# Kernel tuning notes

Hardware: AMD Instinct MI355X
Metric: run time of the kernel (lower is better)

## Reference

```python
import jax, jax.numpy as jnp
import numpy as np

N = 10000      # nodes
E = 160000     # edges
G = 512        # graphs in batch
IN, H, OUT = 128, 512, 16
L = 4          # num_layers
EPS = 1e-5


def setup_inputs() -> dict:
    key = jax.random.key(0)
    ks = jax.random.split(key, 8)
    x = jax.random.normal(ks[0], (N, IN), dtype=jnp.float32)
    edge_index = jax.random.randint(ks[1], (2, E), 0, N)
    batch = jnp.sort(jax.random.randint(ks[2], (N,), 0, G))
    # GCNConv layer 0 (IN -> H) and layers 1..L-1 (H -> H), plus per-layer LayerNorm affine
    W0 = jax.random.normal(ks[3], (IN, H), dtype=jnp.float32) / np.float32(np.sqrt(IN))
    b0 = jnp.zeros((H,), jnp.float32)
    g0 = jnp.ones((IN,), jnp.float32)
    be0 = jnp.zeros((IN,), jnp.float32)
    Wh = jax.random.normal(ks[4], (L - 1, H, H), dtype=jnp.float32) / np.float32(np.sqrt(H))
    bh = jnp.zeros((L - 1, H), jnp.float32)
    gh = jnp.ones((L - 1, H), jnp.float32)
    beh = jnp.zeros((L - 1, H), jnp.float32)
    linW = jax.random.normal(ks[5], (H, OUT), dtype=jnp.float32) / np.float32(np.sqrt(H))
    linb = jnp.zeros((OUT,), jnp.float32)
    return dict(x=x, edge_index=edge_index, batch=batch, W0=W0, b0=b0, g0=g0, be0=be0,
                Wh=Wh, bh=bh, gh=gh, beh=beh, linW=linW, linb=linb)


def _layernorm(x, g, b):
    mu = jnp.mean(x, axis=-1, keepdims=True)
    var = jnp.var(x, axis=-1, keepdims=True)
    return (x - mu) * jax.lax.rsqrt(var + EPS) * g + b


def _gcn(x, W, b, src, dst, dinv):
    # GCNConv with self-loops: out_i = sum_{j->i} d_j^-1/2 d_i^-1/2 (xW)_j + d_i^-1 (xW)_i + b
    h = x @ W                                   # [N, H']
    coef = (dinv[src] * dinv[dst])[:, None]     # [E, 1]
    agg = jax.ops.segment_sum(h[src] * coef, dst, num_segments=N)
    agg = agg + h * (dinv * dinv)[:, None]      # self-loop term
    return agg + b


def reference(x, edge_index, batch, W0, b0, g0, be0, Wh, bh, gh, beh, linW, linb):
    src, dst = edge_index[0], edge_index[1]
    # degree with self-loops (counted on destination nodes, edge weight 1)
    deg = jax.ops.segment_sum(jnp.ones((E,), x.dtype), dst, num_segments=N) + 1.0
    dinv = jax.lax.rsqrt(deg)
    h = jax.nn.relu(_gcn(_layernorm(x, g0, be0), W0, b0, src, dst, dinv))
    for i in range(L - 1):
        h = jax.nn.relu(_gcn(_layernorm(h, gh[i], beh[i]), Wh[i], bh[i], src, dst, dinv))
    # scatter-mean pooling by graph id
    counts = jax.ops.segment_sum(jnp.ones((N,), x.dtype), batch, num_segments=G)
    pooled = jax.ops.segment_sum(h, batch, num_segments=G) / jnp.maximum(counts, 1.0)[:, None]
    return pooled @ linW + linb
```

## Files before the change

kernel.cpp:

```cpp
#include <hip/hip_runtime.h>

#define NN 10000
#define NE 160000
#define NG 512
#define DIN 128
#define DH 512
#define DOUT 16
#define NPAD 10112

typedef __bf16 bf16_t;
typedef __attribute__((ext_vector_type(8))) __bf16 bf16x8;
typedef __attribute__((ext_vector_type(2))) __bf16 bf16x2;
typedef __attribute__((ext_vector_type(4))) float f32x4;
typedef __attribute__((ext_vector_type(2))) float f32x2;

#define LNB 2500
#define DEGB ((NE + 255) / 256)
#define WTE (512 * DIN + 3 * DH * DH)
#define WTB ((WTE + 255) / 256)
#define CURB ((NN + 255) / 256)


__global__ __launch_bounds__(256) void k_prep(const float* __restrict__ x,
                                              const float* __restrict__ g0,
                                              const float* __restrict__ be0,
                                              bf16_t* __restrict__ lnx,
                                              const int* __restrict__ dst,
                                              int* __restrict__ deg,
                                              const float* __restrict__ W0,
                                              const float* __restrict__ Wh,
                                              bf16_t* __restrict__ Wt0,
                                              bf16_t* __restrict__ Wth,
                                              int* __restrict__ cursor) {
    int b = blockIdx.x;
    int tid = threadIdx.x;
    if (b < LNB) {
        int row = b * 4 + (tid >> 6);
        int lane = tid & 63;
        const float* xr = x + (size_t)row * DIN;
        float v0 = xr[lane], v1 = xr[lane + 64];
        float s = v0 + v1, s2 = v0 * v0 + v1 * v1;
#pragma unroll
        for (int off = 32; off; off >>= 1) {
            s += __shfl_xor(s, off);
            s2 += __shfl_xor(s2, off);
        }
        float mu = s * (1.f / 128.f);
        float var = s2 * (1.f / 128.f) - mu * mu;
        float r = rsqrtf(var + 1e-5f);
        bf16_t* yr = lnx + (size_t)row * DIN;
        yr[lane] = (bf16_t)((v0 - mu) * r * g0[lane] + be0[lane]);
        yr[lane + 64] = (bf16_t)((v1 - mu) * r * g0[lane + 64] + be0[lane + 64]);
    } else if (b < LNB + DEGB) {
        int e = (b - LNB) * 256 + tid;
        if (e < NE) atomicAdd(&deg[dst[e]], 1);
    } else if (b < LNB + DEGB + WTB) {
        int idx = (b - LNB - DEGB) * 256 + tid;
        if (idx < 512 * DIN) {
            int k = idx >> 9, n = idx & 511;
            Wt0[n * DIN + k] = (bf16_t)W0[idx];
        } else if (idx < WTE) {
            int j = idx - 512 * DIN;
            int l = j >> 18;
            int r2 = j & 262143;
            int k = r2 >> 9, n = r2 & 511;
            Wth[((size_t)l << 18) + n * DH + k] = (bf16_t)Wh[j];
        }
    } else {
        int i = (b - LNB - DEGB - WTB) * 256 + tid;
        if (i < NN) cursor[i] = 0;
    }
}


__global__ __launch_bounds__(1024) void k_scan(const int* __restrict__ cnt,
                                               int* __restrict__ rowptr,
                                               float* __restrict__ dinv) {
    __shared__ int part[1024];
    int tid = threadIdx.x;
    const int PER = 10;
    int base = tid * PER;
    int local[PER];
    int s = 0;
#pragma unroll
    for (int i = 0; i < PER; ++i) {
        int idx = base + i;
        int v = (idx < NN) ? cnt[idx] : 0;
        if (idx < NN) dinv[idx] = rsqrtf((float)v + 1.0f);
        local[i] = s;
        s += v;
    }
    part[tid] = s;
    __syncthreads();
    for (int off = 1; off < 1024; off <<= 1) {
        int v = (tid >= off) ? part[tid - off] : 0;
        __syncthreads();
        part[tid] += v;
        __syncthreads();
    }
    int offset = (tid > 0) ? part[tid - 1] : 0;
#pragma unroll
    for (int i = 0; i < PER; ++i) {
        int idx = base + i;
        if (idx < NN) rowptr[idx] = offset + local[i];
    }
    if (tid == 1023) rowptr[NN] = part[1023];
}

__global__ void k_fill_csr(const int* __restrict__ src, const int* __restrict__ dst,
                           const float* __restrict__ dinv, const int* __restrict__ rowptr,
                           int* __restrict__ cursor, int2* __restrict__ csr) {
    int e = blockIdx.x * blockDim.x + threadIdx.x;
    if (e >= NE) return;
    int s = src[e], d = dst[e];
    int pos = atomicAdd(&cursor[d], 1);
    csr[rowptr[d] + pos] = make_int2(s, __float_as_int(dinv[s] * dinv[d]));
}


__global__ __launch_bounds__(256) void k_ln512(const bf16_t* __restrict__ x,
                                               const float* __restrict__ g,
                                               const float* __restrict__ b,
                                               bf16_t* __restrict__ y) {
    int row = blockIdx.x * 4 + (threadIdx.x >> 6);
    int lane = threadIdx.x & 63;
    if (row >= NN) return;
    int c0 = lane * 8;
    bf16x8 v = *(const bf16x8*)&x[(size_t)row * DH + c0];
    float f[8];
    float s = 0.f, s2 = 0.f;
#pragma unroll
    for (int i = 0; i < 8; ++i) {
        f[i] = (float)v[i];
        s += f[i];
        s2 += f[i] * f[i];
    }
#pragma unroll
    for (int off = 32; off; off >>= 1) {
        s += __shfl_xor(s, off);
        s2 += __shfl_xor(s2, off);
    }
    float mu = s * (1.f / 512.f);
    float var = s2 * (1.f / 512.f) - mu * mu;
    float r = rsqrtf(var + 1e-5f);
    f32x4 g0 = *(const f32x4*)&g[c0], g1 = *(const f32x4*)&g[c0 + 4];
    f32x4 b0 = *(const f32x4*)&b[c0], b1 = *(const f32x4*)&b[c0 + 4];
    bf16x8 o;
#pragma unroll
    for (int i = 0; i < 4; ++i) {
        o[i] = (bf16_t)((f[i] - mu) * r * g0[i] + b0[i]);
        o[i + 4] = (bf16_t)((f[i + 4] - mu) * r * g1[i] + b1[i]);
    }
    *(bf16x8*)&y[(size_t)row * DH + c0] = o;
}


template <bool EPI>
__global__ __launch_bounds__(256) void k_gemm64(const bf16_t* __restrict__ A,
                                                const bf16_t* __restrict__ Bt,
                                                const float* __restrict__ bias,
                                                bf16_t* __restrict__ C, int K) {
    __shared__ bf16_t As[64 * 64];
    __shared__ bf16_t Bs[64 * 64];
    int tid = threadIdx.x;
    int lane = tid & 63, w = tid >> 6;
    int row0 = blockIdx.x * 64, col0 = blockIdx.y * 64;
    int wm = w >> 1, wn = w & 1;

    f32x4 acc[2][2];
#pragma unroll
    for (int i = 0; i < 2; ++i)
#pragma unroll
        for (int j = 0; j < 2; ++j) acc[i][j] = (f32x4){0.f, 0.f, 0.f, 0.f};

    int lr = lane >> 3;
    int lc = lane & 7;

    for (int kt = 0; kt < K; kt += 64) {
#pragma unroll
        for (int i = 0; i < 2; ++i) {
            int r = w * 16 + i * 8 + lr;
            int cg = lc ^ (r & 7);
            const bf16_t* srca = A + (size_t)(row0 + r) * K + kt + cg * 8;
            __builtin_amdgcn_global_load_lds(
                (const __attribute__((address_space(1))) void*)srca,
                (__attribute__((address_space(3))) void*)(As + (w * 16 + i * 8) * 64),
                16, 0, 0);
            const bf16_t* srcb = Bt + (size_t)(col0 + r) * K + kt + cg * 8;
            __builtin_amdgcn_global_load_lds(
                (const __attribute__((address_space(1))) void*)srcb,
                (__attribute__((address_space(3))) void*)(Bs + (w * 16 + i * 8) * 64),
                16, 0, 0);
        }
        __syncthreads();
#pragma unroll
        for (int ks = 0; ks < 2; ++ks) {
            bf16x8 af[2], bfr[2];
#pragma unroll
            for (int mi = 0; mi < 2; ++mi) {
                int mr = wm * 32 + mi * 16 + (lane & 15);
                int c = (ks * 4 + (lane >> 4)) ^ (mr & 7);
                af[mi] = *(const bf16x8*)&As[mr * 64 + c * 8];
            }
#pragma unroll
            for (int ni = 0; ni < 2; ++ni) {
                int nr = wn * 32 + ni * 16 + (lane & 15);
                int c = (ks * 4 + (lane >> 4)) ^ (nr & 7);
                bfr[ni] = *(const bf16x8*)&Bs[nr * 64 + c * 8];
            }
#pragma unroll
            for (int mi = 0; mi < 2; ++mi)
#pragma unroll
                for (int ni = 0; ni < 2; ++ni)
                    acc[mi][ni] = __builtin_amdgcn_mfma_f32_16x16x32_bf16(
                        af[mi], bfr[ni], acc[mi][ni], 0, 0, 0);
        }
        __syncthreads();
    }
#pragma unroll
    for (int mi = 0; mi < 2; ++mi)
#pragma unroll
        for (int ni = 0; ni < 2; ++ni) {
            int col = col0 + wn * 32 + ni * 16 + (lane & 15);
            float bv = EPI ? bias[col] : 0.f;
#pragma unroll
            for (int q = 0; q < 4; ++q) {
                int row = row0 + wm * 32 + mi * 16 + (lane >> 4) * 4 + q;
                float v = acc[mi][ni][q];
                if (EPI) v = fmaxf(v + bv, 0.f);
                C[(size_t)row * DH + col] = (bf16_t)v;
            }
        }
}


__global__ __launch_bounds__(256) void k_agg128(const bf16_t* __restrict__ H,
                                                const int* __restrict__ rowptr,
                                                const int2* __restrict__ csr,
                                                const float* __restrict__ dinv,
                                                bf16_t* __restrict__ out) {
    __shared__ float part[4][DIN];
    int n = blockIdx.x;
    int w = threadIdx.x >> 6, lane = threadIdx.x & 63;
    int c0 = lane * 2;
    float a0 = 0.f, a1 = 0.f;
    int s0 = rowptr[n], s1 = rowptr[n + 1];
    int k = s0 + w;
    for (; k + 4 < s1; k += 8) {
        int2 eA = csr[k], eB = csr[k + 4];
        float cA = __int_as_float(eA.y), cB = __int_as_float(eB.y);
        bf16x2 vA = *(const bf16x2*)&H[(size_t)eA.x * DIN + c0];
        bf16x2 vB = *(const bf16x2*)&H[(size_t)eB.x * DIN + c0];
        a0 += (float)vA[0] * cA + (float)vB[0] * cB;
        a1 += (float)vA[1] * cA + (float)vB[1] * cB;
    }
    if (k < s1) {
        int2 eA = csr[k];
        float cA = __int_as_float(eA.y);
        bf16x2 vA = *(const bf16x2*)&H[(size_t)eA.x * DIN + c0];
        a0 += (float)vA[0] * cA;
        a1 += (float)vA[1] * cA;
    }
    part[w][c0] = a0;
    part[w][c0 + 1] = a1;
    __syncthreads();
    if (threadIdx.x < 64) {
        int cc = threadIdx.x * 2;
        float b0 = part[0][cc] + part[1][cc] + part[2][cc] + part[3][cc];
        float b1 = part[0][cc + 1] + part[1][cc + 1] + part[2][cc + 1] + part[3][cc + 1];
        float di = dinv[n], sc = di * di;
        bf16x2 vs = *(const bf16x2*)&H[(size_t)n * DIN + cc];
        b0 += (float)vs[0] * sc;
        b1 += (float)vs[1] * sc;
        bf16x2 o;
        o[0] = (bf16_t)b0;
        o[1] = (bf16_t)b1;
        *(bf16x2*)&out[(size_t)n * DIN + cc] = o;
    }
}


template <bool DO_LN>
__global__ __launch_bounds__(256) void k_agg(const bf16_t* __restrict__ H,
                                             const int* __restrict__ rowptr,
                                             const int2* __restrict__ csr,
                                             const float* __restrict__ dinv,
                                             const float* __restrict__ bias,
                                             const float* __restrict__ gamma,
                                             const float* __restrict__ beta,
                                             bf16_t* __restrict__ out) {
    __shared__ float part[4][DH];
    __shared__ float rs[8];
    int n = blockIdx.x;
    int w = threadIdx.x >> 6, lane = threadIdx.x & 63;
    int c0 = lane * 8;
    float acc[8] = {0.f, 0.f, 0.f, 0.f, 0.f, 0.f, 0.f, 0.f};
    int s0 = rowptr[n], s1 = rowptr[n + 1];
    int k = s0 + w;
    for (; k + 4 < s1; k += 8) {
        int2 eA = csr[k], eB = csr[k + 4];
        float cA = __int_as_float(eA.y), cB = __int_as_float(eB.y);
        bf16x8 vA = *(const bf16x8*)&H[(size_t)eA.x * DH + c0];
        bf16x8 vB = *(const bf16x8*)&H[(size_t)eB.x * DH + c0];
#pragma unroll
        for (int i = 0; i < 8; ++i) acc[i] += (float)vA[i] * cA + (float)vB[i] * cB;
    }
    if (k < s1) {
        int2 eA = csr[k];
        float cA = __int_as_float(eA.y);
        bf16x8 vA = *(const bf16x8*)&H[(size_t)eA.x * DH + c0];
#pragma unroll
        for (int i = 0; i < 8; ++i) acc[i] += (float)vA[i] * cA;
    }
    *(f32x4*)&part[w][c0] = (f32x4){acc[0], acc[1], acc[2], acc[3]};
    *(f32x4*)&part[w][c0 + 4] = (f32x4){acc[4], acc[5], acc[6], acc[7]};
    __syncthreads();
    int cc = threadIdx.x * 2;
    f32x2 p0 = *(const f32x2*)&part[0][cc];
    f32x2 p1 = *(const f32x2*)&part[1][cc];
    f32x2 p2 = *(const f32x2*)&part[2][cc];
    f32x2 p3 = *(const f32x2*)&part[3][cc];
    float a0 = p0[0] + p1[0] + p2[0] + p3[0];
    float a1 = p0[1] + p1[1] + p2[1] + p3[1];
    float di = dinv[n], sc = di * di;
    bf16x2 vs = *(const bf16x2*)&H[(size_t)n * DH + cc];
    a0 += (float)vs[0] * sc;
    a1 += (float)vs[1] * sc;
    a0 = fmaxf(a0 + bias[cc], 0.f);
    a1 = fmaxf(a1 + bias[cc + 1], 0.f);
    bf16x2 o;
    if (DO_LN) {
        float s = a0 + a1, s2 = a0 * a0 + a1 * a1;
#pragma unroll
        for (int off = 32; off; off >>= 1) {
            s += __shfl_xor(s, off);
            s2 += __shfl_xor(s2, off);
        }
        if (lane == 0) {
            rs[w] = s;
            rs[4 + w] = s2;
        }
        __syncthreads();
        s = rs[0] + rs[1] + rs[2] + rs[3];
        s2 = rs[4] + rs[5] + rs[6] + rs[7];
        float mu = s * (1.f / 512.f);
        float var = s2 * (1.f / 512.f) - mu * mu;
        float r = rsqrtf(var + 1e-5f);
        o[0] = (bf16_t)((a0 - mu) * r * gamma[cc] + beta[cc]);
        o[1] = (bf16_t)((a1 - mu) * r * gamma[cc + 1] + beta[cc + 1]);
    } else {
        o[0] = (bf16_t)a0;
        o[1] = (bf16_t)a1;
    }
    *(bf16x2*)&out[(size_t)n * DH + cc] = o;
}


__global__ __launch_bounds__(256) void k_poolfin(const bf16_t* __restrict__ h,
                                                 const int* __restrict__ batch,
                                                 const float* __restrict__ linW,
                                                 const float* __restrict__ linb,
                                                 float* __restrict__ out) {
    __shared__ float pooled[DH];
    __shared__ float red[256];
    int g = blockIdx.x;
    int t = threadIdx.x;
    int lo = 0, hi = NN;
    while (lo < hi) {
        int mid = (lo + hi) >> 1;
        if (batch[mid] < g) lo = mid + 1;
        else hi = mid;
    }
    int start = lo;
    hi = NN;
    while (lo < hi) {
        int mid = (lo + hi) >> 1;
        if (batch[mid] < g + 1) lo = mid + 1;
        else hi = mid;
    }
    int end = lo;
    int c0 = t * 2;
    float a0 = 0.f, a1 = 0.f;
    for (int i = start; i < end; ++i) {
        bf16x2 v = *(const bf16x2*)&h[(size_t)i * DH + c0];
        a0 += (float)v[0];
        a1 += (float)v[1];
    }
    float inv = 1.f / fmaxf((float)(end - start), 1.0f);
    pooled[c0] = a0 * inv;
    pooled[c0 + 1] = a1 * inv;
    __syncthreads();
    int o = t & 15, c = t >> 4;
    float s = 0.f;
    int k0 = c * 32;
    for (int k = k0; k < k0 + 32; ++k) s += pooled[k] * linW[k * DOUT + o];
    red[t] = s;
    __syncthreads();
    if (t < DOUT) {
        float acc2 = 0.f;
        for (int cc = 0; cc < 16; ++cc) acc2 += red[cc * 16 + t];
        out[g * DOUT + t] = acc2 + linb[t];
    }
}


extern "C" void kernel_launch(void* const* d_in, const int* in_sizes, int n_in,
                              void* d_out, int out_size, void* d_ws, size_t ws_size,
                              hipStream_t stream) {
    const float* x = (const float*)d_in[0];
    const int* ei = (const int*)d_in[1];
    const int* batch = (const int*)d_in[2];
    const float* W0 = (const float*)d_in[3];
    const float* b0 = (const float*)d_in[4];
    const float* g0 = (const float*)d_in[5];
    const float* be0 = (const float*)d_in[6];
    const float* Wh = (const float*)d_in[7];
    const float* bh = (const float*)d_in[8];
    const float* gh = (const float*)d_in[9];
    const float* beh = (const float*)d_in[10];
    const float* linW = (const float*)d_in[11];
    const float* linb = (const float*)d_in[12];
    float* out = (float*)d_out;

    bf16_t* lnbuf = (bf16_t*)d_ws;
    bf16_t* Cbf = lnbuf + (size_t)NPAD * DH;
    bf16_t* lnx = Cbf + (size_t)NPAD * DH;
    bf16_t* aggx = lnx + (size_t)NPAD * DIN;
    bf16_t* Wt0 = aggx + (size_t)NPAD * DIN;
    bf16_t* Wth = Wt0 + 512 * DIN;
    float* dinv = (float*)(Wth + 3 * DH * DH);
    int* deg = (int*)(dinv + NN);
    int* rowptr = deg + NN;
    int* cursor = rowptr + NN + 1;
    int2* csr = (int2*)(cursor + NN + 1);

    const int* srcp = ei;
    const int* dstp = ei + NE;

    hipMemsetAsync(deg, 0, NN * sizeof(int), stream);
    k_prep<<<LNB + DEGB + WTB + CURB, 256, 0, stream>>>(x, g0, be0, lnx, dstp, deg,
                                                        W0, Wh, Wt0, Wth, cursor);
    k_scan<<<1, 1024, 0, stream>>>(deg, rowptr, dinv);
    k_fill_csr<<<(NE + 255) / 256, 256, 0, stream>>>(srcp, dstp, dinv, rowptr, cursor, csr);

    dim3 gemm_grid(NPAD / 64, DH / 64);

    k_agg128<<<NN, 256, 0, stream>>>(lnx, rowptr, csr, dinv, aggx);
    k_gemm64<true><<<gemm_grid, 256, 0, stream>>>(aggx, Wt0, b0, Cbf, DIN);
    k_ln512<<<(NN + 3) / 4, 256, 0, stream>>>(Cbf, gh + 0 * DH, beh + 0 * DH, lnbuf);

    for (int l = 0; l < 2; ++l) {
        k_gemm64<false><<<gemm_grid, 256, 0, stream>>>(lnbuf, Wth + (size_t)l * DH * DH,
                                                       nullptr, Cbf, DH);
        k_agg<true><<<NN, 256, 0, stream>>>(Cbf, rowptr, csr, dinv, bh + l * DH,
                                            gh + (l + 1) * DH, beh + (l + 1) * DH, lnbuf);
    }
    k_gemm64<false><<<gemm_grid, 256, 0, stream>>>(lnbuf, Wth + (size_t)2 * DH * DH,
                                                   nullptr, Cbf, DH);
    k_agg<false><<<NN, 256, 0, stream>>>(Cbf, rowptr, csr, dinv, bh + 2 * DH,
                                         nullptr, nullptr, lnbuf);

    k_poolfin<<<NG, 256, 0, stream>>>(lnbuf, batch, linW, linb, out);
}
```

Measured before the change: 207.4 us.

## Fuse final aggregation with pooling, enlarge GEMM tile, and optimise scan and gather unroll

The last aggregation now scatter-adds its ReLU outputs straight into a per-graph pooled buffer with float atomics, so the separate sequential pooling pass over node rows is gone. The buffer is zeroed by extra blocks in the prep kernel. The GEMM tile grows from 64x64 to 128x64 to get more reuse per block, at the cost of fewer blocks. The single-block scan switches from a shared-memory Hillis-Steele loop to wave shuffles, and the edge-gather loops unroll by four instead of two. The atomics make the pooled sums order-nondeterministic.

```diff
diff --git a/kernel.cpp b/kernel.cpp
--- a/kernel.cpp
+++ b/kernel.cpp
@@ -19,6 +19,7 @@
 #define WTE (512 * DIN + 3 * DH * DH)
 #define WTB ((WTE + 255) / 256)
 #define CURB ((NN + 255) / 256)
+#define PLB 256
 
 
 __global__ __launch_bounds__(256) void k_prep(const float* __restrict__ x,
@@ -31,7 +32,8 @@
                                               const float* __restrict__ Wh,
                                               bf16_t* __restrict__ Wt0,
                                               bf16_t* __restrict__ Wth,
-                                              int* __restrict__ cursor) {
+                                              int* __restrict__ cursor,
+                                              float* __restrict__ pooled) {
     int b = blockIdx.x;
     int tid = threadIdx.x;
     if (b < LNB) {
@@ -66,9 +68,12 @@
             int k = r2 >> 9, n = r2 & 511;
             Wth[((size_t)l << 18) + n * DH + k] = (bf16_t)Wh[j];
         }
-    } else {
+    } else if (b < LNB + DEGB + WTB + CURB) {
         int i = (b - LNB - DEGB - WTB) * 256 + tid;
         if (i < NN) cursor[i] = 0;
+    } else {
+        int i = (b - LNB - DEGB - WTB - CURB) * 256 + tid;
+        ((f32x4*)pooled)[i] = (f32x4){0.f, 0.f, 0.f, 0.f};
     }
 }
 
@@ -76,8 +81,8 @@
 __global__ __launch_bounds__(1024) void k_scan(const int* __restrict__ cnt,
                                                int* __restrict__ rowptr,
                                                float* __restrict__ dinv) {
-    __shared__ int part[1024];
-    int tid = threadIdx.x;
+    __shared__ int wsum[16];
+    int tid = threadIdx.x, lane = tid & 63, wid = tid >> 6;
     const int PER = 10;
     int base = tid * PER;
     int local[PER];
@@ -90,21 +95,32 @@
         local[i] = s;
         s += v;
     }
-    part[tid] = s;
-    __syncthreads();
-    for (int off = 1; off < 1024; off <<= 1) {
-        int v = (tid >= off) ? part[tid - off] : 0;
-        __syncthreads();
-        part[tid] += v;
-        __syncthreads();
-    }
-    int offset = (tid > 0) ? part[tid - 1] : 0;
+    int mysum = s;
+#pragma unroll
+    for (int off = 1; off < 64; off <<= 1) {
+        int v = __shfl_up(s, off);
+        if (lane >= off) s += v;
+    }
+    if (lane == 63) wsum[wid] = s;
+    __syncthreads();
+    if (tid < 16) {
+        int v = wsum[tid];
+#pragma unroll
+        for (int off = 1; off < 16; off <<= 1) {
+            int u = __shfl_up(v, off);
+            if (lane >= off) v += u;
+        }
+        wsum[tid] = v;
+    }
+    __syncthreads();
+    int woff = (wid > 0) ? wsum[wid - 1] : 0;
+    int excl = s - mysum + woff;
 #pragma unroll
     for (int i = 0; i < PER; ++i) {
         int idx = base + i;
-        if (idx < NN) rowptr[idx] = offset + local[i];
-    }
-    if (tid == 1023) rowptr[NN] = part[1023];
+        if (idx < NN) rowptr[idx] = excl + local[i];
+    }
+    if (tid == 1023) rowptr[NN] = excl + mysum;
 }
 
 __global__ void k_fill_csr(const int* __restrict__ src, const int* __restrict__ dst,
@@ -156,20 +172,21 @@
 
 
 template <bool EPI>
-__global__ __launch_bounds__(256) void k_gemm64(const bf16_t* __restrict__ A,
-                                                const bf16_t* __restrict__ Bt,
-                                                const float* __restrict__ bias,
-                                                bf16_t* __restrict__ C, int K) {
-    __shared__ bf16_t As[64 * 64];
+__global__ __launch_bounds__(256) void k_gemm_bf16(const bf16_t* __restrict__ A,
+                                                   const bf16_t* __restrict__ Bt,
+                                                   const float* __restrict__ bias,
+                                                   bf16_t* __restrict__ C, int K) {
+    __shared__ bf16_t As[128 * 64];
     __shared__ bf16_t Bs[64 * 64];
     int tid = threadIdx.x;
     int lane = tid & 63, w = tid >> 6;
-    int row0 = blockIdx.x * 64, col0 = blockIdx.y * 64;
+    int row0 = blockIdx.x * 128;
+    int col0 = blockIdx.y * 64;
     int wm = w >> 1, wn = w & 1;
 
-    f32x4 acc[2][2];
-#pragma unroll
-    for (int i = 0; i < 2; ++i)
+    f32x4 acc[4][2];
+#pragma unroll
+    for (int i = 0; i < 4; ++i)
 #pragma unroll
         for (int j = 0; j < 2; ++j) acc[i][j] = (f32x4){0.f, 0.f, 0.f, 0.f};
 
@@ -177,28 +194,33 @@
     int lc = lane & 7;
 
     for (int kt = 0; kt < K; kt += 64) {
+#pragma unroll
+        for (int i = 0; i < 4; ++i) {
+            int r = w * 32 + i * 8 + lr;
+            int cg = lc ^ (r & 7);
+            const bf16_t* src = A + (size_t)(row0 + r) * K + kt + cg * 8;
+            __builtin_amdgcn_global_load_lds(
+                (const __attribute__((address_space(1))) void*)src,
+                (__attribute__((address_space(3))) void*)(As + (w * 32 + i * 8) * 64),
+                16, 0, 0);
+        }
 #pragma unroll
         for (int i = 0; i < 2; ++i) {
             int r = w * 16 + i * 8 + lr;
             int cg = lc ^ (r & 7);
-            const bf16_t* srca = A + (size_t)(row0 + r) * K + kt + cg * 8;
+            const bf16_t* src = Bt + (size_t)(col0 + r) * K + kt + cg * 8;
             __builtin_amdgcn_global_load_lds(
-                (const __attribute__((address_space(1))) void*)srca,
-                (__attribute__((address_space(3))) void*)(As + (w * 16 + i * 8) * 64),
-                16, 0, 0);
-            const bf16_t* srcb = Bt + (size_t)(col0 + r) * K + kt + cg * 8;
-            __builtin_amdgcn_global_load_lds(
-                (const __attribute__((address_space(1))) void*)srcb,
+                (const __attribute__((address_space(1))) void*)src,
                 (__attribute__((address_space(3))) void*)(Bs + (w * 16 + i * 8) * 64),
                 16, 0, 0);
         }
         __syncthreads();
 #pragma unroll
         for (int ks = 0; ks < 2; ++ks) {
-            bf16x8 af[2], bfr[2];
-#pragma unroll
-            for (int mi = 0; mi < 2; ++mi) {
-                int mr = wm * 32 + mi * 16 + (lane & 15);
+            bf16x8 af[4], bfr[2];
+#pragma unroll
+            for (int mi = 0; mi < 4; ++mi) {
+                int mr = wm * 64 + mi * 16 + (lane & 15);
                 int c = (ks * 4 + (lane >> 4)) ^ (mr & 7);
                 af[mi] = *(const bf16x8*)&As[mr * 64 + c * 8];
             }
@@ -209,7 +231,7 @@
                 bfr[ni] = *(const bf16x8*)&Bs[nr * 64 + c * 8];
             }
 #pragma unroll
-            for (int mi = 0; mi < 2; ++mi)
+            for (int mi = 0; mi < 4; ++mi)
 #pragma unroll
                 for (int ni = 0; ni < 2; ++ni)
                     acc[mi][ni] = __builtin_amdgcn_mfma_f32_16x16x32_bf16(
@@ -218,14 +240,14 @@
         __syncthreads();
     }
 #pragma unroll
-    for (int mi = 0; mi < 2; ++mi)
+    for (int mi = 0; mi < 4; ++mi)
 #pragma unroll
         for (int ni = 0; ni < 2; ++ni) {
             int col = col0 + wn * 32 + ni * 16 + (lane & 15);
             float bv = EPI ? bias[col] : 0.f;
 #pragma unroll
             for (int q = 0; q < 4; ++q) {
-                int row = row0 + wm * 32 + mi * 16 + (lane >> 4) * 4 + q;
+                int row = row0 + wm * 64 + mi * 16 + (lane >> 4) * 4 + q;
                 float v = acc[mi][ni][q];
                 if (EPI) v = fmaxf(v + bv, 0.f);
                 C[(size_t)row * DH + col] = (bf16_t)v;
@@ -246,15 +268,18 @@
     float a0 = 0.f, a1 = 0.f;
     int s0 = rowptr[n], s1 = rowptr[n + 1];
     int k = s0 + w;
-    for (; k + 4 < s1; k += 8) {
-        int2 eA = csr[k], eB = csr[k + 4];
-        float cA = __int_as_float(eA.y), cB = __int_as_float(eB.y);
-        bf16x2 vA = *(const bf16x2*)&H[(size_t)eA.x * DIN + c0];
-        bf16x2 vB = *(const bf16x2*)&H[(size_t)eB.x * DIN + c0];
-        a0 += (float)vA[0] * cA + (float)vB[0] * cB;
-        a1 += (float)vA[1] * cA + (float)vB[1] * cB;
-    }
-    if (k < s1) {
+    for (; k + 12 < s1; k += 16) {
+        int2 e0 = csr[k], e1 = csr[k + 4], e2 = csr[k + 8], e3 = csr[k + 12];
+        bf16x2 v0 = *(const bf16x2*)&H[(size_t)e0.x * DIN + c0];
+        bf16x2 v1 = *(const bf16x2*)&H[(size_t)e1.x * DIN + c0];
+        bf16x2 v2 = *(const bf16x2*)&H[(size_t)e2.x * DIN + c0];
+        bf16x2 v3 = *(const bf16x2*)&H[(size_t)e3.x * DIN + c0];
+        float c0f = __int_as_float(e0.y), c1f = __int_as_float(e1.y);
+        float c2f = __int_as_float(e2.y), c3f = __int_as_float(e3.y);
+        a0 += (float)v0[0] * c0f + (float)v1[0] * c1f + (float)v2[0] * c2f + (float)v3[0] * c3f;
+        a1 += (float)v0[1] * c0f + (float)v1[1] * c1f + (float)v2[1] * c2f + (float)v3[1] * c3f;
+    }
+    for (; k < s1; k += 4) {
         int2 eA = csr[k];
         float cA = __int_as_float(eA.y);
         bf16x2 vA = *(const bf16x2*)&H[(size_t)eA.x * DIN + c0];
@@ -280,15 +305,42 @@
 }
 
 
-template <bool DO_LN>
-__global__ __launch_bounds__(256) void k_agg(const bf16_t* __restrict__ H,
-                                             const int* __restrict__ rowptr,
-                                             const int2* __restrict__ csr,
-                                             const float* __restrict__ dinv,
-                                             const float* __restrict__ bias,
-                                             const float* __restrict__ gamma,
-                                             const float* __restrict__ beta,
-                                             bf16_t* __restrict__ out) {
+__device__ __forceinline__ void agg_core(const bf16_t* __restrict__ H,
+                                         const int2* __restrict__ csr,
+                                         int s0, int s1, int w, int c0,
+                                         float* __restrict__ acc) {
+    int k = s0 + w;
+    for (; k + 12 < s1; k += 16) {
+        int2 e0 = csr[k], e1 = csr[k + 4], e2 = csr[k + 8], e3 = csr[k + 12];
+        bf16x8 v0 = *(const bf16x8*)&H[(size_t)e0.x * DH + c0];
+        bf16x8 v1 = *(const bf16x8*)&H[(size_t)e1.x * DH + c0];
+        bf16x8 v2 = *(const bf16x8*)&H[(size_t)e2.x * DH + c0];
+        bf16x8 v3 = *(const bf16x8*)&H[(size_t)e3.x * DH + c0];
+        float c0f = __int_as_float(e0.y), c1f = __int_as_float(e1.y);
+        float c2f = __int_as_float(e2.y), c3f = __int_as_float(e3.y);
+#pragma unroll
+        for (int i = 0; i < 8; ++i)
+            acc[i] += (float)v0[i] * c0f + (float)v1[i] * c1f +
+                      (float)v2[i] * c2f + (float)v3[i] * c3f;
+    }
+    for (; k < s1; k += 4) {
+        int2 eA = csr[k];
+        float cA = __int_as_float(eA.y);
+        bf16x8 vA = *(const bf16x8*)&H[(size_t)eA.x * DH + c0];
+#pragma unroll
+        for (int i = 0; i < 8; ++i) acc[i] += (float)vA[i] * cA;
+    }
+}
+
+
+__global__ __launch_bounds__(256) void k_agg_ln(const bf16_t* __restrict__ H,
+                                                const int* __restrict__ rowptr,
+                                                const int2* __restrict__ csr,
+                                                const float* __restrict__ dinv,
+                                                const float* __restrict__ bias,
+                                                const float* __restrict__ gamma,
+                                                const float* __restrict__ beta,
+                                                bf16_t* __restrict__ out) {
     __shared__ float part[4][DH];
     __shared__ float rs[8];
     int n = blockIdx.x;
@@ -296,22 +348,7 @@
     int c0 = lane * 8;
     float acc[8] = {0.f, 0.f, 0.f, 0.f, 0.f, 0.f, 0.f, 0.f};
     int s0 = rowptr[n], s1 = rowptr[n + 1];
-    int k = s0 + w;
-    for (; k + 4 < s1; k += 8) {
-        int2 eA = csr[k], eB = csr[k + 4];
-        float cA = __int_as_float(eA.y), cB = __int_as_float(eB.y);
-        bf16x8 vA = *(const bf16x8*)&H[(size_t)eA.x * DH + c0];
-        bf16x8 vB = *(const bf16x8*)&H[(size_t)eB.x * DH + c0];
-#pragma unroll
-        for (int i = 0; i < 8; ++i) acc[i] += (float)vA[i] * cA + (float)vB[i] * cB;
-    }
-    if (k < s1) {
-        int2 eA = csr[k];
-        float cA = __int_as_float(eA.y);
-        bf16x8 vA = *(const bf16x8*)&H[(size_t)eA.x * DH + c0];
-#pragma unroll
-        for (int i = 0; i < 8; ++i) acc[i] += (float)vA[i] * cA;
-    }
+    agg_core(H, csr, s0, s1, w, c0, acc);
     *(f32x4*)&part[w][c0] = (f32x4){acc[0], acc[1], acc[2], acc[3]};
     *(f32x4*)&part[w][c0 + 4] = (f32x4){acc[4], acc[5], acc[6], acc[7]};
     __syncthreads();
@@ -328,40 +365,72 @@
     a1 += (float)vs[1] * sc;
     a0 = fmaxf(a0 + bias[cc], 0.f);
     a1 = fmaxf(a1 + bias[cc + 1], 0.f);
+    float s = a0 + a1, s2 = a0 * a0 + a1 * a1;
+#pragma unroll
+    for (int off = 32; off; off >>= 1) {
+        s += __shfl_xor(s, off);
+        s2 += __shfl_xor(s2, off);
+    }
+    if (lane == 0) {
+        rs[w] = s;
+        rs[4 + w] = s2;
+    }
+    __syncthreads();
+    s = rs[0] + rs[1] + rs[2] + rs[3];
+    s2 = rs[4] + rs[5] + rs[6] + rs[7];
+    float mu = s * (1.f / 512.f);
+    float var = s2 * (1.f / 512.f) - mu * mu;
+    float r = rsqrtf(var + 1e-5f);
     bf16x2 o;
-    if (DO_LN) {
-        float s = a0 + a1, s2 = a0 * a0 + a1 * a1;
-#pragma unroll
-        for (int off = 32; off; off >>= 1) {
-            s += __shfl_xor(s, off);
-            s2 += __shfl_xor(s2, off);
-        }
-        if (lane == 0) {
-            rs[w] = s;
-            rs[4 + w] = s2;
-        }
-        __syncthreads();
-        s = rs[0] + rs[1] + rs[2] + rs[3];
-        s2 = rs[4] + rs[5] + rs[6] + rs[7];
-        float mu = s * (1.f / 512.f);
-        float var = s2 * (1.f / 512.f) - mu * mu;
-        float r = rsqrtf(var + 1e-5f);
-        o[0] = (bf16_t)((a0 - mu) * r * gamma[cc] + beta[cc]);
-        o[1] = (bf16_t)((a1 - mu) * r * gamma[cc + 1] + beta[cc + 1]);
-    } else {
-        o[0] = (bf16_t)a0;
-        o[1] = (bf16_t)a1;
-    }
+    o[0] = (bf16_t)((a0 - mu) * r * gamma[cc] + beta[cc]);
+    o[1] = (bf16_t)((a1 - mu) * r * gamma[cc + 1] + beta[cc + 1]);
     *(bf16x2*)&out[(size_t)n * DH + cc] = o;
 }
 
 
-__global__ __launch_bounds__(256) void k_poolfin(const bf16_t* __restrict__ h,
-                                                 const int* __restrict__ batch,
-                                                 const float* __restrict__ linW,
-                                                 const float* __restrict__ linb,
-                                                 float* __restrict__ out) {
-    __shared__ float pooled[DH];
+__global__ __launch_bounds__(256) void k_agg_pool(const bf16_t* __restrict__ H,
+                                                  const int* __restrict__ rowptr,
+                                                  const int2* __restrict__ csr,
+                                                  const float* __restrict__ dinv,
+                                                  const float* __restrict__ bias,
+                                                  const int* __restrict__ batch,
+                                                  float* __restrict__ pooled) {
+    __shared__ float part[4][DH];
+    int n = blockIdx.x;
+    int w = threadIdx.x >> 6, lane = threadIdx.x & 63;
+    int c0 = lane * 8;
+    float acc[8] = {0.f, 0.f, 0.f, 0.f, 0.f, 0.f, 0.f, 0.f};
+    int s0 = rowptr[n], s1 = rowptr[n + 1];
+    agg_core(H, csr, s0, s1, w, c0, acc);
+    *(f32x4*)&part[w][c0] = (f32x4){acc[0], acc[1], acc[2], acc[3]};
+    *(f32x4*)&part[w][c0 + 4] = (f32x4){acc[4], acc[5], acc[6], acc[7]};
+    __syncthreads();
+    int cc = threadIdx.x * 2;
+    f32x2 p0 = *(const f32x2*)&part[0][cc];
+    f32x2 p1 = *(const f32x2*)&part[1][cc];
+    f32x2 p2 = *(const f32x2*)&part[2][cc];
+    f32x2 p3 = *(const f32x2*)&part[3][cc];
+    float a0 = p0[0] + p1[0] + p2[0] + p3[0];
+    float a1 = p0[1] + p1[1] + p2[1] + p3[1];
+    float di = dinv[n], sc = di * di;
+    bf16x2 vs = *(const bf16x2*)&H[(size_t)n * DH + cc];
+    a0 += (float)vs[0] * sc;
+    a1 += (float)vs[1] * sc;
+    a0 = fmaxf(a0 + bias[cc], 0.f);
+    a1 = fmaxf(a1 + bias[cc + 1], 0.f);
+    int g = batch[n];
+    float* dstp = pooled + (size_t)g * DH + cc;
+    atomicAdd(dstp, a0);
+    atomicAdd(dstp + 1, a1);
+}
+
+
+__global__ __launch_bounds__(256) void k_fin(const float* __restrict__ pooled,
+                                             const int* __restrict__ batch,
+                                             const float* __restrict__ linW,
+                                             const float* __restrict__ linb,
+                                             float* __restrict__ out) {
+    __shared__ float prow[DH];
     __shared__ float red[256];
     int g = blockIdx.x;
     int t = threadIdx.x;
@@ -379,26 +448,21 @@
         else hi = mid;
     }
     int end = lo;
-    int c0 = t * 2;
-    float a0 = 0.f, a1 = 0.f;
-    for (int i = start; i < end; ++i) {
-        bf16x2 v = *(const bf16x2*)&h[(size_t)i * DH + c0];
-        a0 += (float)v[0];
-        a1 += (float)v[1];
-    }
     float inv = 1.f / fmaxf((float)(end - start), 1.0f);
-    pooled[c0] = a0 * inv;
-    pooled[c0 + 1] = a1 * inv;
+    int cc = t * 2;
+    f32x2 pv = *(const f32x2*)&pooled[(size_t)g * DH + cc];
+    prow[cc] = pv[0] * inv;
+    prow[cc + 1] = pv[1] * inv;
     __syncthreads();
     int o = t & 15, c = t >> 4;
     float s = 0.f;
     int k0 = c * 32;
-    for (int k = k0; k < k0 + 32; ++k) s += pooled[k] * linW[k * DOUT + o];
+    for (int k = k0; k < k0 + 32; ++k) s += prow[k] * linW[k * DOUT + o];
     red[t] = s;
     __syncthreads();
     if (t < DOUT) {
         float acc2 = 0.f;
-        for (int cc = 0; cc < 16; ++cc) acc2 += red[cc * 16 + t];
+        for (int ccq = 0; ccq < 16; ++ccq) acc2 += red[ccq * 16 + t];
         out[g * DOUT + t] = acc2 + linb[t];
     }
 }
@@ -428,7 +492,8 @@
     bf16_t* aggx = lnx + (size_t)NPAD * DIN;
     bf16_t* Wt0 = aggx + (size_t)NPAD * DIN;
     bf16_t* Wth = Wt0 + 512 * DIN;
-    float* dinv = (float*)(Wth + 3 * DH * DH);
+    float* pooled = (float*)(Wth + 3 * DH * DH);
+    float* dinv = pooled + (size_t)NG * DH;
     int* deg = (int*)(dinv + NN);
     int* rowptr = deg + NN;
     int* cursor = rowptr + NN + 1;
@@ -438,27 +503,26 @@
     const int* dstp = ei + NE;
 
     hipMemsetAsync(deg, 0, NN * sizeof(int), stream);
-    k_prep<<<LNB + DEGB + WTB + CURB, 256, 0, stream>>>(x, g0, be0, lnx, dstp, deg,
-                                                        W0, Wh, Wt0, Wth, cursor);
+    k_prep<<<LNB + DEGB + WTB + CURB + PLB, 256, 0, stream>>>(
+        x, g0, be0, lnx, dstp, deg, W0, Wh, Wt0, Wth, cursor, pooled);
     k_scan<<<1, 1024, 0, stream>>>(deg, rowptr, dinv);
     k_fill_csr<<<(NE + 255) / 256, 256, 0, stream>>>(srcp, dstp, dinv, rowptr, cursor, csr);
 
-    dim3 gemm_grid(NPAD / 64, DH / 64);
+    dim3 gemm_grid(NPAD / 128, DH / 64);
 
     k_agg128<<<NN, 256, 0, stream>>>(lnx, rowptr, csr, dinv, aggx);
-    k_gemm64<true><<<gemm_grid, 256, 0, stream>>>(aggx, Wt0, b0, Cbf, DIN);
+    k_gemm_bf16<true><<<gemm_grid, 256, 0, stream>>>(aggx, Wt0, b0, Cbf, DIN);
     k_ln512<<<(NN + 3) / 4, 256, 0, stream>>>(Cbf, gh + 0 * DH, beh + 0 * DH, lnbuf);
 
     for (int l = 0; l < 2; ++l) {
-        k_gemm64<false><<<gemm_grid, 256, 0, stream>>>(lnbuf, Wth + (size_t)l * DH * DH,
-                                                       nullptr, Cbf, DH);
-        k_agg<true><<<NN, 256, 0, stream>>>(Cbf, rowptr, csr, dinv, bh + l * DH,
-                                            gh + (l + 1) * DH, beh + (l + 1) * DH, lnbuf);
-    }
-    k_gemm64<false><<<gemm_grid, 256, 0, stream>>>(lnbuf, Wth + (size_t)2 * DH * DH,
-                                                   nullptr, Cbf, DH);
-    k_agg<false><<<NN, 256, 0, stream>>>(Cbf, rowptr, csr, dinv, bh + 2 * DH,
-                                         nullptr, nullptr, lnbuf);
-
-    k_poolfin<<<NG, 256, 0, stream>>>(lnbuf, batch, linW, linb, out);
-}
+        k_gemm_bf16<false><<<gemm_grid, 256, 0, stream>>>(lnbuf, Wth + (size_t)l * DH * DH,
+                                                          nullptr, Cbf, DH);
+        k_agg_ln<<<NN, 256, 0, stream>>>(Cbf, rowptr, csr, dinv, bh + l * DH,
+                                         gh + (l + 1) * DH, beh + (l + 1) * DH, lnbuf);
+    }
+    k_gemm_bf16<false><<<gemm_grid, 256, 0, stream>>>(lnbuf, Wth + (size_t)2 * DH * DH,
+                                                      nullptr, Cbf, DH);
+    k_agg_pool<<<NN, 256, 0, stream>>>(Cbf, rowptr, csr, dinv, bh + 2 * DH, batch, pooled);
+
+    k_fin<<<NG, 256, 0, stream>>>(pooled, batch, linW, linb, out);
+}
```

Result: slower. 229.8 us (+10.8%).
